# Kernel tuning notes

Hardware: AMD Instinct MI355X
Metric: run time of the kernel (lower is better)

The kernel has to match this reference:

```python
import jax, jax.numpy as jnp
import numpy as np

HID, OUT, VOC, MEM, MDIM, OPN = 2048, 4096, 4096, 4096, 64, 5

def setup_inputs() -> dict:
    key = jax.random.key(0)
    ks = jax.random.split(key, 16)
    s = 0.02
    return {
        "input": jax.random.normal(ks[0], (1, 1, VOC), jnp.float32),
        "hidden0": jax.random.normal(ks[1], (1, 1, HID), jnp.float32),
        "memory": jax.random.normal(ks[2], (MEM, MDIM), jnp.float32),
        "W_ih": jax.random.normal(ks[3], (HID, VOC), jnp.float32) * s,
        "b_ih": jax.random.normal(ks[4], (HID,), jnp.float32) * s,
        "W_hh": jax.random.normal(ks[5], (HID, HID), jnp.float32) * s,
        "b_hh": jax.random.normal(ks[6], (HID,), jnp.float32) * s,
        "Wm_w": jax.random.normal(ks[7], (HID, MDIM), jnp.float32) * s,
        "Wm_b": jax.random.normal(ks[8], (HID,), jnp.float32) * s,
        "Wy_w": jax.random.normal(ks[9], (OUT, HID), jnp.float32) * s,
        "Wy_b": jax.random.normal(ks[10], (OUT,), jnp.float32) * s,
        "Wn_w": jax.random.normal(ks[11], (MDIM, HID), jnp.float32) * s,
        "Wn_b": jax.random.normal(ks[12], (MDIM,), jnp.float32) * s,
        "Wa_w": jax.random.normal(ks[13], (OPN, HID), jnp.float32) * s,
        "Wa_b": jax.random.normal(ks[14], (OPN,), jnp.float32) * s,
    }

def reference(input, hidden0, memory, W_ih, b_ih, W_hh, b_hh, Wm_w, Wm_b,
              Wy_w, Wy_b, Wn_w, Wn_b, Wa_w, Wa_b):
    # hidden_bar = W_m(memory[0]) + hidden0 ; shapes: (HID,)
    h_bar = memory[0] @ Wm_w.T + Wm_b + hidden0[0, 0]
    # single-step, single-layer tanh RNN
    x = input[0, 0]  # (VOC,)
    h = jnp.tanh(x @ W_ih.T + b_ih + h_bar @ W_hh.T + b_hh)  # (HID,)
    ht = h.reshape(1, 1, HID)
    output = jax.nn.sigmoid(h @ Wy_w.T + Wy_b).reshape(1, 1, OUT)
    a = jax.nn.softmax(h @ Wa_w.T + Wa_b)  # (5,) action weights
    new_elt = jax.nn.sigmoid(h @ Wn_w.T + Wn_b)  # (MDIM,)
    # Permutation matmuls expressed as exact index shifts:
    left = jnp.roll(memory, -1, axis=0)          # leftmove @ memory
    right = jnp.roll(memory, 1, axis=0)          # rightmove @ memory
    leftinv = right.at[0].set(0.0)               # rightmove with row 0 zeroed
    rightinv = left.at[MEM - 1].set(0.0)         # leftmove with last row zeroed
    mem = (left * a[0] + right * a[1] + memory * a[2]
           + leftinv * a[3] + rightinv * a[4])
    # simple_addition @ new_elt adds new_elt into row 0 only
    mem = mem.at[0].add(new_elt)
    return (output, ht, mem)
```

## Files before the change

### kernel.cpp

```cpp
#include <hip/hip_runtime.h>
#include <hip/hip_bf16.h>

#define HID 2048
#define OUTN 4096
#define VOC 4096
#define MEMN 4096
#define MDIM 64
#define OPN 5

static __device__ __forceinline__ float wave_reduce(float v) {
    #pragma unroll
    for (int off = 32; off > 0; off >>= 1) v += __shfl_down(v, off, 64);
    return v;
}

static __device__ __forceinline__ float block_reduce(float v, float* red) {
    int lane = threadIdx.x & 63;
    int wid = threadIdx.x >> 6;
    v = wave_reduce(v);
    if (lane == 0) red[wid] = v;
    __syncthreads();
    return red[0] + red[1] + red[2] + red[3];
}

__global__ __launch_bounds__(256) void k_hbar(
        const float* __restrict__ Wm_w,
        const float* __restrict__ Wm_b,
        const float* __restrict__ memory,
        const float* __restrict__ hidden0,
        float* __restrict__ h_bar) {
    int wave = (blockIdx.x * blockDim.x + threadIdx.x) >> 6;
    int lane = threadIdx.x & 63;
    if (wave >= HID) return;
    float v = Wm_w[(size_t)wave * MDIM + lane] * memory[lane];
    v = wave_reduce(v);
    if (lane == 0)
        h_bar[wave] = v + Wm_b[wave] + hidden0[wave];
}

__global__ __launch_bounds__(256) void k_hidden(
        const float* __restrict__ W_ih,
        const float* __restrict__ x,
        const float* __restrict__ b_ih,
        const float* __restrict__ W_hh,
        const float* __restrict__ b_hh,
        const float* __restrict__ h_bar,
        float* __restrict__ h,
        float* __restrict__ ht_out) {
    __shared__ float red[4];
    int row = blockIdx.x;
    int tid = threadIdx.x;
    float acc = 0.f;
    const float* wrow = W_ih + (size_t)row * VOC;
    #pragma unroll
    for (int p = 0; p < VOC / (256 * 4); ++p) {
        int k = (p * 256 + tid) * 4;
        float4 w = *(const float4*)(wrow + k);
        float4 xv = *(const float4*)(x + k);
        acc += w.x * xv.x + w.y * xv.y + w.z * xv.z + w.w * xv.w;
    }
    const float* wrow2 = W_hh + (size_t)row * HID;
    #pragma unroll
    for (int p = 0; p < HID / (256 * 4); ++p) {
        int k = (p * 256 + tid) * 4;
        float4 w = *(const float4*)(wrow2 + k);
        float4 hv = *(const float4*)(h_bar + k);
        acc += w.x * hv.x + w.y * hv.y + w.z * hv.z + w.w * hv.w;
    }
    float s = block_reduce(acc, red);
    if (tid == 0) {
        float hv = tanhf(s + b_ih[row] + b_hh[row]);
        h[row] = hv;
        ht_out[row] = hv;
    }
}

__global__ __launch_bounds__(256) void k_heads(
        const float* __restrict__ Wy_w,
        const float* __restrict__ Wy_b,
        const float* __restrict__ Wn_w,
        const float* __restrict__ Wn_b,
        const float* __restrict__ Wa_w,
        const float* __restrict__ Wa_b,
        const float* __restrict__ h,
        float* __restrict__ out,
        float* __restrict__ new_elt,
        float* __restrict__ wa_logits) {
    __shared__ float red[4];
    int row = blockIdx.x;
    int tid = threadIdx.x;
    const float* wrow;
    if (row < OUTN)             wrow = Wy_w + (size_t)row * HID;
    else if (row < OUTN + MDIM) wrow = Wn_w + (size_t)(row - OUTN) * HID;
    else                        wrow = Wa_w + (size_t)(row - OUTN - MDIM) * HID;
    float acc = 0.f;
    #pragma unroll
    for (int p = 0; p < HID / (256 * 4); ++p) {
        int k = (p * 256 + tid) * 4;
        float4 w = *(const float4*)(wrow + k);
        float4 hv = *(const float4*)(h + k);
        acc += w.x * hv.x + w.y * hv.y + w.z * hv.z + w.w * hv.w;
    }
    float s = block_reduce(acc, red);
    if (tid == 0) {
        if (row < OUTN) {
            float v = s + Wy_b[row];
            out[row] = 1.f / (1.f + expf(-v));
        } else if (row < OUTN + MDIM) {
            int r = row - OUTN;
            float v = s + Wn_b[r];
            new_elt[r] = 1.f / (1.f + expf(-v));
        } else {
            int r = row - OUTN - MDIM;
            wa_logits[r] = s + Wa_b[r];
        }
    }
}

__global__ __launch_bounds__(256) void k_mem(
        const float* __restrict__ m,
        const float* __restrict__ wa,
        const float* __restrict__ new_elt,
        float* __restrict__ mem_out) {
    int idx = blockIdx.x * blockDim.x + threadIdx.x;
    if (idx >= MEMN * MDIM) return;
    float l0 = wa[0], l1 = wa[1], l2 = wa[2], l3 = wa[3], l4 = wa[4];
    float mx = fmaxf(fmaxf(fmaxf(l0, l1), fmaxf(l2, l3)), l4);
    float e0 = expf(l0 - mx), e1 = expf(l1 - mx), e2 = expf(l2 - mx),
          e3 = expf(l3 - mx), e4 = expf(l4 - mx);
    float inv = 1.f / (e0 + e1 + e2 + e3 + e4);
    float a0 = e0 * inv, a1 = e1 * inv, a2 = e2 * inv, a3 = e3 * inv, a4 = e4 * inv;

    int r = idx >> 6, c = idx & (MDIM - 1);
    float mc = m[idx];
    float mp = m[(size_t)((r + 1) & (MEMN - 1)) * MDIM + c];
    float mm = m[(size_t)((r - 1) & (MEMN - 1)) * MDIM + c];
    float cp = a0 + (r < MEMN - 1 ? a4 : 0.f);
    float cm = a1 + (r > 0 ? a3 : 0.f);
    float v = cp * mp + cm * mm + a2 * mc;
    if (r == 0) v += new_elt[c];
    mem_out[idx] = v;
}

extern "C" void kernel_launch(void* const* d_in, const int* in_sizes, int n_in,
                              void* d_out, int out_size, void* d_ws, size_t ws_size,
                              hipStream_t stream) {
    const float* input   = (const float*)d_in[0];
    const float* hidden0 = (const float*)d_in[1];
    const float* memory  = (const float*)d_in[2];
    const float* W_ih    = (const float*)d_in[3];
    const float* b_ih    = (const float*)d_in[4];
    const float* W_hh    = (const float*)d_in[5];
    const float* b_hh    = (const float*)d_in[6];
    const float* Wm_w    = (const float*)d_in[7];
    const float* Wm_b    = (const float*)d_in[8];
    const float* Wy_w    = (const float*)d_in[9];
    const float* Wy_b    = (const float*)d_in[10];
    const float* Wn_w    = (const float*)d_in[11];
    const float* Wn_b    = (const float*)d_in[12];
    const float* Wa_w    = (const float*)d_in[13];
    const float* Wa_b    = (const float*)d_in[14];

    float* ws      = (float*)d_ws;
    float* h_bar   = ws;
    float* h       = ws + 2048;
    float* wa      = ws + 4096;
    float* new_elt = ws + 4104;

    float* out_f = (float*)d_out;
    float* ht_f  = (float*)d_out + OUTN;
    float* mem_f = (float*)d_out + OUTN + HID;

    k_hbar<<<HID / 4, 256, 0, stream>>>(Wm_w, Wm_b, memory, hidden0, h_bar);
    k_hidden<<<HID, 256, 0, stream>>>(W_ih, input, b_ih, W_hh, b_hh,
                                      h_bar, h, ht_f);
    int rows3 = OUTN + MDIM + OPN;
    k_heads<<<rows3, 256, 0, stream>>>(Wy_w, Wy_b, Wn_w, Wn_b,
                                       Wa_w, Wa_b, h, out_f,
                                       new_elt, wa);
    k_mem<<<(MEMN * MDIM) / 256, 256, 0, stream>>>(memory, wa, new_elt, mem_f);
}
```

Measured before the change: 138.0 us.

## Fuse all four stages into one cooperative kernel with grid syncs

Replaces the four separate launches (h_bar, hidden RNN step, output heads, memory update) with a single cooperative kernel of 512 blocks. Grid-wide syncs separate the stages, so each block now handles several rows per stage. The memory update is also vectorised to float2 loads and stores. The aim is to remove launch overhead and inter-kernel gaps, at the cost of grid-sync latency and fewer blocks in flight for the bandwidth-bound GEMV stages.

```diff
diff --git a/kernel.cpp b/kernel.cpp
--- a/kernel.cpp
+++ b/kernel.cpp
@@ -1,5 +1,7 @@
 #include <hip/hip_runtime.h>
-#include <hip/hip_bf16.h>
+#include <hip/hip_cooperative_groups.h>
+
+namespace cg = cooperative_groups;
 
 #define HID 2048
 #define OUTN 4096
@@ -7,6 +9,7 @@
 #define MEMN 4096
 #define MDIM 64
 #define OPN 5
+#define NBLK 512
 
 static __device__ __forceinline__ float wave_reduce(float v) {
     #pragma unroll
@@ -23,123 +26,129 @@
     return red[0] + red[1] + red[2] + red[3];
 }
 
-__global__ __launch_bounds__(256) void k_hbar(
-        const float* __restrict__ Wm_w,
-        const float* __restrict__ Wm_b,
+__global__ __launch_bounds__(256) void mega(
+        const float* __restrict__ input,
+        const float* __restrict__ hidden0,
         const float* __restrict__ memory,
-        const float* __restrict__ hidden0,
-        float* __restrict__ h_bar) {
-    int wave = (blockIdx.x * blockDim.x + threadIdx.x) >> 6;
-    int lane = threadIdx.x & 63;
-    if (wave >= HID) return;
-    float v = Wm_w[(size_t)wave * MDIM + lane] * memory[lane];
-    v = wave_reduce(v);
-    if (lane == 0)
-        h_bar[wave] = v + Wm_b[wave] + hidden0[wave];
-}
-
-__global__ __launch_bounds__(256) void k_hidden(
         const float* __restrict__ W_ih,
-        const float* __restrict__ x,
         const float* __restrict__ b_ih,
         const float* __restrict__ W_hh,
         const float* __restrict__ b_hh,
-        const float* __restrict__ h_bar,
-        float* __restrict__ h,
-        float* __restrict__ ht_out) {
-    __shared__ float red[4];
-    int row = blockIdx.x;
-    int tid = threadIdx.x;
-    float acc = 0.f;
-    const float* wrow = W_ih + (size_t)row * VOC;
-    #pragma unroll
-    for (int p = 0; p < VOC / (256 * 4); ++p) {
-        int k = (p * 256 + tid) * 4;
-        float4 w = *(const float4*)(wrow + k);
-        float4 xv = *(const float4*)(x + k);
-        acc += w.x * xv.x + w.y * xv.y + w.z * xv.z + w.w * xv.w;
-    }
-    const float* wrow2 = W_hh + (size_t)row * HID;
-    #pragma unroll
-    for (int p = 0; p < HID / (256 * 4); ++p) {
-        int k = (p * 256 + tid) * 4;
-        float4 w = *(const float4*)(wrow2 + k);
-        float4 hv = *(const float4*)(h_bar + k);
-        acc += w.x * hv.x + w.y * hv.y + w.z * hv.z + w.w * hv.w;
-    }
-    float s = block_reduce(acc, red);
-    if (tid == 0) {
-        float hv = tanhf(s + b_ih[row] + b_hh[row]);
-        h[row] = hv;
-        ht_out[row] = hv;
-    }
-}
-
-__global__ __launch_bounds__(256) void k_heads(
+        const float* __restrict__ Wm_w,
+        const float* __restrict__ Wm_b,
         const float* __restrict__ Wy_w,
         const float* __restrict__ Wy_b,
         const float* __restrict__ Wn_w,
         const float* __restrict__ Wn_b,
         const float* __restrict__ Wa_w,
         const float* __restrict__ Wa_b,
-        const float* __restrict__ h,
-        float* __restrict__ out,
-        float* __restrict__ new_elt,
-        float* __restrict__ wa_logits) {
+        float* __restrict__ out_f,
+        float* __restrict__ ht_f,
+        float* __restrict__ mem_f,
+        float* __restrict__ ws) {
+    cg::grid_group grid = cg::this_grid();
     __shared__ float red[4];
-    int row = blockIdx.x;
-    int tid = threadIdx.x;
-    const float* wrow;
-    if (row < OUTN)             wrow = Wy_w + (size_t)row * HID;
-    else if (row < OUTN + MDIM) wrow = Wn_w + (size_t)(row - OUTN) * HID;
-    else                        wrow = Wa_w + (size_t)(row - OUTN - MDIM) * HID;
-    float acc = 0.f;
+    const int tid = threadIdx.x;
+    const int bid = blockIdx.x;
+
+    float* h_bar   = ws;
+    float* h       = ws + 2048;
+    float* wa      = ws + 4096;
+    float* new_elt = ws + 4104;
+
+    {
+        int wid = tid >> 6, lane = tid & 63;
+        int row = bid * 4 + wid;
+        float v = Wm_w[(size_t)row * MDIM + lane] * memory[lane];
+        v = wave_reduce(v);
+        if (lane == 0) h_bar[row] = v + Wm_b[row] + hidden0[row];
+    }
+    grid.sync();
+
     #pragma unroll
-    for (int p = 0; p < HID / (256 * 4); ++p) {
-        int k = (p * 256 + tid) * 4;
-        float4 w = *(const float4*)(wrow + k);
-        float4 hv = *(const float4*)(h + k);
-        acc += w.x * hv.x + w.y * hv.y + w.z * hv.z + w.w * hv.w;
+    for (int i = 0; i < 4; ++i) {
+        int row = bid * 4 + i;
+        float acc = 0.f;
+        const float* wrow = W_ih + (size_t)row * VOC;
+        #pragma unroll
+        for (int p = 0; p < VOC / (256 * 4); ++p) {
+            int k = (p * 256 + tid) * 4;
+            float4 w = *(const float4*)(wrow + k);
+            float4 xv = *(const float4*)(input + k);
+            acc += w.x * xv.x + w.y * xv.y + w.z * xv.z + w.w * xv.w;
+        }
+        const float* wrow2 = W_hh + (size_t)row * HID;
+        #pragma unroll
+        for (int p = 0; p < HID / (256 * 4); ++p) {
+            int k = (p * 256 + tid) * 4;
+            float4 w = *(const float4*)(wrow2 + k);
+            float4 hv = *(const float4*)(h_bar + k);
+            acc += w.x * hv.x + w.y * hv.y + w.z * hv.z + w.w * hv.w;
+        }
+        float s = block_reduce(acc, red);
+        if (tid == 0) {
+            float hv = tanhf(s + b_ih[row] + b_hh[row]);
+            h[row] = hv;
+            ht_f[row] = hv;
+        }
+        __syncthreads();
     }
-    float s = block_reduce(acc, red);
-    if (tid == 0) {
-        if (row < OUTN) {
-            float v = s + Wy_b[row];
-            out[row] = 1.f / (1.f + expf(-v));
-        } else if (row < OUTN + MDIM) {
-            int r = row - OUTN;
-            float v = s + Wn_b[r];
-            new_elt[r] = 1.f / (1.f + expf(-v));
-        } else {
-            int r = row - OUTN - MDIM;
-            wa_logits[r] = s + Wa_b[r];
+    grid.sync();
+
+    for (int row = bid; row < OUTN + MDIM + OPN; row += NBLK) {
+        const float* wrow;
+        if (row < OUTN)             wrow = Wy_w + (size_t)row * HID;
+        else if (row < OUTN + MDIM) wrow = Wn_w + (size_t)(row - OUTN) * HID;
+        else                        wrow = Wa_w + (size_t)(row - OUTN - MDIM) * HID;
+        float acc = 0.f;
+        #pragma unroll
+        for (int p = 0; p < HID / (256 * 4); ++p) {
+            int k = (p * 256 + tid) * 4;
+            float4 w = *(const float4*)(wrow + k);
+            float4 hv = *(const float4*)(h + k);
+            acc += w.x * hv.x + w.y * hv.y + w.z * hv.z + w.w * hv.w;
         }
+        float s = block_reduce(acc, red);
+        if (tid == 0) {
+            if (row < OUTN) {
+                float v = s + Wy_b[row];
+                out_f[row] = 1.f / (1.f + expf(-v));
+            } else if (row < OUTN + MDIM) {
+                int r = row - OUTN;
+                float v = s + Wn_b[r];
+                new_elt[r] = 1.f / (1.f + expf(-v));
+            } else {
+                int r = row - OUTN - MDIM;
+                wa[r] = s + Wa_b[r];
+            }
+        }
+        __syncthreads();
     }
-}
+    grid.sync();
 
-__global__ __launch_bounds__(256) void k_mem(
-        const float* __restrict__ m,
-        const float* __restrict__ wa,
-        const float* __restrict__ new_elt,
-        float* __restrict__ mem_out) {
-    int idx = blockIdx.x * blockDim.x + threadIdx.x;
-    if (idx >= MEMN * MDIM) return;
-    float l0 = wa[0], l1 = wa[1], l2 = wa[2], l3 = wa[3], l4 = wa[4];
-    float mx = fmaxf(fmaxf(fmaxf(l0, l1), fmaxf(l2, l3)), l4);
-    float e0 = expf(l0 - mx), e1 = expf(l1 - mx), e2 = expf(l2 - mx),
-          e3 = expf(l3 - mx), e4 = expf(l4 - mx);
-    float inv = 1.f / (e0 + e1 + e2 + e3 + e4);
-    float a0 = e0 * inv, a1 = e1 * inv, a2 = e2 * inv, a3 = e3 * inv, a4 = e4 * inv;
+    {
+        float l0 = wa[0], l1 = wa[1], l2 = wa[2], l3 = wa[3], l4 = wa[4];
+        float mx = fmaxf(fmaxf(fmaxf(l0, l1), fmaxf(l2, l3)), l4);
+        float e0 = expf(l0 - mx), e1 = expf(l1 - mx), e2 = expf(l2 - mx),
+              e3 = expf(l3 - mx), e4 = expf(l4 - mx);
+        float inv = 1.f / (e0 + e1 + e2 + e3 + e4);
+        float a0 = e0 * inv, a1 = e1 * inv, a2 = e2 * inv,
+              a3 = e3 * inv, a4 = e4 * inv;
 
-    int r = idx >> 6, c = idx & (MDIM - 1);
-    float mc = m[idx];
-    float mp = m[(size_t)((r + 1) & (MEMN - 1)) * MDIM + c];
-    float mm = m[(size_t)((r - 1) & (MEMN - 1)) * MDIM + c];
-    float cp = a0 + (r < MEMN - 1 ? a4 : 0.f);
-    float cm = a1 + (r > 0 ? a3 : 0.f);
-    float v = cp * mp + cm * mm + a2 * mc;
-    if (r == 0) v += new_elt[c];
-    mem_out[idx] = v;
+        int t = bid * 256 + tid;
+        int idx = t * 2;
+        int r = idx >> 6, c = idx & (MDIM - 1);
+        float2 mc = *(const float2*)(memory + (size_t)r * MDIM + c);
+        float2 mp = *(const float2*)(memory + (size_t)((r + 1) & (MEMN - 1)) * MDIM + c);
+        float2 mm = *(const float2*)(memory + (size_t)((r - 1) & (MEMN - 1)) * MDIM + c);
+        float cp = a0 + (r < MEMN - 1 ? a4 : 0.f);
+        float cm = a1 + (r > 0 ? a3 : 0.f);
+        float2 v;
+        v.x = cp * mp.x + cm * mm.x + a2 * mc.x;
+        v.y = cp * mp.y + cm * mm.y + a2 * mc.y;
+        if (r == 0) { v.x += new_elt[c]; v.y += new_elt[c + 1]; }
+        *(float2*)(mem_f + idx) = v;
+    }
 }
 
 extern "C" void kernel_launch(void* const* d_in, const int* in_sizes, int n_in,
@@ -161,22 +170,18 @@
     const float* Wa_w    = (const float*)d_in[13];
     const float* Wa_b    = (const float*)d_in[14];
 
-    float* ws      = (float*)d_ws;
-    float* h_bar   = ws;
-    float* h       = ws + 2048;
-    float* wa      = ws + 4096;
-    float* new_elt = ws + 4104;
-
+    float* ws    = (float*)d_ws;
     float* out_f = (float*)d_out;
     float* ht_f  = (float*)d_out + OUTN;
     float* mem_f = (float*)d_out + OUTN + HID;
 
-    k_hbar<<<HID / 4, 256, 0, stream>>>(Wm_w, Wm_b, memory, hidden0, h_bar);
-    k_hidden<<<HID, 256, 0, stream>>>(W_ih, input, b_ih, W_hh, b_hh,
-                                      h_bar, h, ht_f);
-    int rows3 = OUTN + MDIM + OPN;
-    k_heads<<<rows3, 256, 0, stream>>>(Wy_w, Wy_b, Wn_w, Wn_b,
-                                       Wa_w, Wa_b, h, out_f,
-                                       new_elt, wa);
-    k_mem<<<(MEMN * MDIM) / 256, 256, 0, stream>>>(memory, wa, new_elt, mem_f);
+    void* args[] = {
+        (void*)&input, (void*)&hidden0, (void*)&memory,
+        (void*)&W_ih, (void*)&b_ih, (void*)&W_hh, (void*)&b_hh,
+        (void*)&Wm_w, (void*)&Wm_b, (void*)&Wy_w, (void*)&Wy_b,
+        (void*)&Wn_w, (void*)&Wn_b, (void*)&Wa_w, (void*)&Wa_b,
+        (void*)&out_f, (void*)&ht_f, (void*)&mem_f, (void*)&ws,
+    };
+    hipLaunchCooperativeKernel((void*)mega, dim3(NBLK), dim3(256),
+                               args, 0, stream);
 }
```

Measured after the change: 317.6 us. +130.2%, slower.
